# Kernel tuning notes

Measured on AMD Instinct MI355X. Metric: run time of the kernel, lower is better.

The kernel has to match this reference:

```python
import jax, jax.numpy as jnp
import numpy as np

B, S, DIM = 2, 4096, 768
G = DIM // 3          # gate_dim = 256
H, DK = 4, G // 4     # heads=4, d_k=64
SCALE = 1.0 / np.sqrt(DK)


def setup_inputs() -> dict:
    key = jax.random.key(0)
    ks = jax.random.split(key, 9)
    r = lambda k, shp, s: (jax.random.normal(k, shp, dtype=jnp.float32) * s)
    w_s = 1.0 / np.sqrt(G)
    return {
        "x": r(ks[0], (B, S, DIM), 1.0),
        "wq": r(ks[1], (G, G), w_s), "bq": r(ks[2], (G,), 0.01),
        "wk": r(ks[3], (G, G), w_s), "bk": r(ks[4], (G,), 0.01),
        "wv": r(ks[5], (G, G), w_s), "bv": r(ks[6], (G,), 0.01),
        "wo": r(ks[7], (G, G), w_s), "bo": r(ks[8], (G,), 0.01),
    }


def reference(x, wq, bq, wk, bk, wv, bv, wo, bo):
    # chunk(3, dim=-1): q/k/v slices of width G
    xq, xk, xv = x[..., :G], x[..., G:2 * G], x[..., 2 * G:3 * G]
    # linear projections then split into heads: [b, s, h, d]
    q = (xq @ wq.T + bq).reshape(B, S, H, DK)
    k = (xk @ wk.T + bk).reshape(B, S, H, DK)
    v = (xv @ wv.T + bv).reshape(B, S, H, DK)
    scores = jnp.einsum('bihd,bjhd->bijh', q, k) * SCALE  # [b, i, j, h]
    # NOTE: original applies Softmax(dim=1) -> over the QUERY axis i
    attn = jax.nn.softmax(scores, axis=1)
    out = jnp.einsum('bijh,bjhd->bihd', attn, v).reshape(B, S, G)
    return out @ wo.T + bo
```

## Files before the change

kernel.cpp:

```cpp
#include <hip/hip_runtime.h>

#define SEQ   4096
#define HH    4
#define SCALE 0.125f

typedef __bf16 bf16x8 __attribute__((ext_vector_type(8)));
typedef __bf16 bf16x4 __attribute__((ext_vector_type(4)));
typedef float  f32x4  __attribute__((ext_vector_type(4)));

constexpr size_t OFF_W16  = 0;
constexpr size_t OFF_A    = 131072;
constexpr size_t OFF_PZ   = 163840;
constexpr size_t OFF_AO   = 294912;
constexpr size_t OFF_X16  = 9732096;
constexpr size_t OFF_Q16  = 12877824;
constexpr size_t K16OFF   = 2097152;
constexpr size_t V16OFF   = 4194304;

__device__ __forceinline__ f32x4 mf(bf16x8 a, bf16x8 b, f32x4 c) {
    return __builtin_amdgcn_mfma_f32_16x16x32_bf16(a, b, c, 0, 0, 0);
}

__device__ __forceinline__ void gload16(const __bf16* g, __bf16* l) {
    __builtin_amdgcn_global_load_lds(
        (const __attribute__((address_space(1))) unsigned int*)g,
        (__attribute__((address_space(3))) unsigned int*)l, 16, 0, 0);
}

__global__ void k_prep(const float* __restrict__ x,
                       const float* __restrict__ wq, const float* __restrict__ wk,
                       const float* __restrict__ wv, const float* __restrict__ wo,
                       float* __restrict__ ws) {
    int bx = blockIdx.x, t = threadIdx.x;
    if (bx < 6144) {
        size_t i4 = ((size_t)bx * 256 + t) * 4;
        float4 v = *(const float4*)(x + i4);
        bf16x4 o = {(__bf16)v.x, (__bf16)v.y, (__bf16)v.z, (__bf16)v.w};
        *(bf16x4*)((__bf16*)(ws + OFF_X16) + i4) = o;
    } else if (bx < 6400) {
        int q = bx - 6144;
        int y = q >> 6;
        const float* src = (y == 0) ? wq : (y == 1) ? wk : (y == 2) ? wv : wo;
        size_t i4 = ((size_t)(q & 63) * 256 + t) * 4;
        float4 v = *(const float4*)(src + i4);
        bf16x4 o = {(__bf16)v.x, (__bf16)v.y, (__bf16)v.z, (__bf16)v.w};
        *(bf16x4*)((__bf16*)(ws + OFF_W16) + (size_t)y * 65536 + i4) = o;
    } else {
        size_t i4 = ((size_t)(bx - 6400) * 256 + t) * 4;
        *(float4*)(ws + OFF_AO + i4) = make_float4(0.f, 0.f, 0.f, 0.f);
    }
}

__global__ __launch_bounds__(256) void k_qkv_mfma(const float* __restrict__ bq,
                                                  const float* __restrict__ bk,
                                                  const float* __restrict__ bv,
                                                  float* __restrict__ ws) {
    int t = threadIdx.x, lane = t & 63, w = t >> 6;
    int yw = blockIdx.y;
    int row0 = blockIdx.x * 64 + w * 16;
    int mrow = lane & 15, quad = lane >> 4;
    const __bf16* X16 = (const __bf16*)(ws + OFF_X16);
    const __bf16* W16 = (const __bf16*)(ws + OFF_W16) + (size_t)yw * 65536;
    const float* bias = (yw == 0) ? bq : (yw == 1) ? bk : bv;
    __bf16* Qb = (__bf16*)(ws + OFF_Q16);
    f32x4 acc[16];
#pragma unroll
    for (int n = 0; n < 16; n++) acc[n] = {0.f, 0.f, 0.f, 0.f};
    const __bf16* ap = X16 + (size_t)(row0 + mrow) * 768 + yw * 256 + quad * 8;
    const __bf16* bp = W16 + (size_t)mrow * 256 + quad * 8;
    for (int kc = 0; kc < 256; kc += 32) {
        bf16x8 a = *(const bf16x8*)(ap + kc);
#pragma unroll
        for (int nt = 0; nt < 16; nt++) {
            bf16x8 b = *(const bf16x8*)(bp + (size_t)nt * 16 * 256 + kc);
            acc[nt] = mf(a, b, acc[nt]);
        }
    }
#pragma unroll
    for (int nt = 0; nt < 16; nt++) {
        int n = nt * 16 + mrow;
        float bb = bias[n];
        int h = n >> 6, d = n & 63;
#pragma unroll
        for (int r = 0; r < 4; r++) {
            int sg = row0 + quad * 4 + r;
            int b_ = sg >> 12, s = sg & 4095;
            int bh = b_ * HH + h;
            float val = acc[nt][r] + bb;
            if (yw <= 1) {
                int tile = s >> 4, m = s & 15, frag = d >> 5, q2 = (d >> 3) & 3, e = d & 7;
                size_t idx = (((size_t)bh * 256 + tile) * 2 + frag) * 512 +
                             (size_t)(q2 * 16 + m) * 8 + e;
                ((yw == 0) ? Qb : Qb + K16OFF)[idx] = (__bf16)val;
            } else {
                int jc = s >> 5, qk = (s >> 3) & 3, e = s & 7;
                int nd = d >> 4, nl = d & 15;
                size_t idx = (((size_t)bh * 128 + jc) * 4 + nd) * 512 +
                             (size_t)(qk * 16 + nl) * 8 + e;
                Qb[V16OFF + idx] = (__bf16)val;
            }
        }
    }
}

__global__ __launch_bounds__(256) void k_colstats(float* __restrict__ ws) {
    __shared__ __bf16 qbuf[2][4096];
    int t = threadIdx.x, lane = t & 63, w = t >> 6;
    int jb = blockIdx.x, iy = blockIdx.y, bh = blockIdx.z;
    int jt0 = jb * 8 + w * 2;
    const __bf16* Qp = (const __bf16*)(ws + OFF_Q16);
    const __bf16* Kp = Qp + K16OFF;
    const __bf16* kb = Kp + (((size_t)bh * 256 + jt0) * 2) * 512 + lane * 8;
    bf16x8 bk00 = *(const bf16x8*)(kb);
    bf16x8 bk01 = *(const bf16x8*)(kb + 512);
    bf16x8 bk10 = *(const bf16x8*)(kb + 1024);
    bf16x8 bk11 = *(const bf16x8*)(kb + 1536);
    const __bf16* q0 = Qp + (((size_t)bh * 256 + iy * 64) * 2) * 512 +
                       w * 1024 + lane * 8;
    gload16(q0, qbuf[0] + w * 1024);
    gload16(q0 + 512, qbuf[0] + w * 1024 + 512);
    __syncthreads();
    float z0 = 0.f, z1 = 0.f;
    for (int ic = 0; ic < 16; ic++) {
        const __bf16* cur = qbuf[ic & 1];
        if (ic < 15) {
            const __bf16* qn = Qp + (((size_t)bh * 256 + iy * 64 + (ic + 1) * 4) * 2) * 512 +
                               w * 1024 + lane * 8;
            gload16(qn, qbuf[(ic + 1) & 1] + w * 1024);
            gload16(qn + 512, qbuf[(ic + 1) & 1] + w * 1024 + 512);
        }
#pragma unroll
        for (int it = 0; it < 4; it++) {
            bf16x8 a0 = *(const bf16x8*)(cur + it * 1024 + lane * 8);
            bf16x8 a1 = *(const bf16x8*)(cur + it * 1024 + 512 + lane * 8);
            f32x4 c0 = {0.f, 0.f, 0.f, 0.f};
            c0 = mf(a0, bk00, c0);
            c0 = mf(a1, bk01, c0);
            f32x4 c1 = {0.f, 0.f, 0.f, 0.f};
            c1 = mf(a0, bk10, c1);
            c1 = mf(a1, bk11, c1);
#pragma unroll
            for (int r = 0; r < 4; r++) {
                z0 += __expf(fmaf(c0[r], SCALE, -16.0f));
                z1 += __expf(fmaf(c1[r], SCALE, -16.0f));
            }
        }
        __syncthreads();
    }
    z0 += __shfl_xor(z0, 16, 64);
    z0 += __shfl_xor(z0, 32, 64);
    z1 += __shfl_xor(z1, 16, 64);
    z1 += __shfl_xor(z1, 32, 64);
    if (lane < 16) {
        size_t o = OFF_PZ + (size_t)iy * 32768 + (size_t)bh * SEQ + jt0 * 16 + lane;
        ws[o] = z0;
        ws[o + 16] = z1;
    }
}

__global__ void k_afin(float* __restrict__ ws) {
    int idx = blockIdx.x * 256 + threadIdx.x;
    const float* pz = ws + OFF_PZ;
    float Z = pz[idx] + pz[32768 + (size_t)idx] + pz[65536 + (size_t)idx] +
              pz[98304 + (size_t)idx];
    ws[OFF_A + idx] = -16.0f - __logf(Z);
}

__global__ __launch_bounds__(256) void k_attnpv(float* __restrict__ ws) {
    __shared__ __bf16 ldsK[2][2048], ldsV[2][2048], ptile[4 * 1280];
    int t = threadIdx.x, lane = t & 63, w = t >> 6;
    int jy = blockIdx.y, bh = blockIdx.z;
    int it0 = blockIdx.x * 8 + w * 2;
    int mrow = lane & 15, quad = lane >> 4;
    const __bf16* Qp = (const __bf16*)(ws + OFF_Q16);
    const __bf16* Kp = Qp + K16OFF;
    const __bf16* Vp = Qp + V16OFF;
    const float* Ac = ws + OFF_A + (size_t)bh * SEQ;
    __bf16* pt = ptile + w * 1280;

    const __bf16* qb = Qp + (((size_t)bh * 256 + it0) * 2) * 512 + lane * 8;
    bf16x8 aq00 = *(const bf16x8*)(qb);
    bf16x8 aq01 = *(const bf16x8*)(qb + 512);
    bf16x8 aq10 = *(const bf16x8*)(qb + 1024);
    bf16x8 aq11 = *(const bf16x8*)(qb + 1536);

    f32x4 oacc[2][4];
#pragma unroll
    for (int tt = 0; tt < 2; tt++)
#pragma unroll
        for (int nd = 0; nd < 4; nd++) oacc[tt][nd] = {0.f, 0.f, 0.f, 0.f};

    int jbase = jy * 1024;
    {
        const __bf16* kg = Kp + (((size_t)bh * 256 + (jbase >> 4)) * 2) * 512 +
                           w * 512 + lane * 8;
        gload16(kg, ldsK[0] + w * 512);
        const __bf16* vg = Vp + (((size_t)bh * 128 + (jbase >> 5)) * 4) * 512 +
                           w * 512 + lane * 8;
        gload16(vg, ldsV[0] + w * 512);
    }
    __syncthreads();

    for (int jt = 0; jt < 32; jt++) {
        int j0 = jbase + jt * 32;
        const __bf16* curK = ldsK[jt & 1];
        const __bf16* curV = ldsV[jt & 1];
        if (jt < 31) {
            int jn = j0 + 32;
            const __bf16* kg = Kp + (((size_t)bh * 256 + (jn >> 4)) * 2) * 512 +
                               w * 512 + lane * 8;
            gload16(kg, ldsK[(jt + 1) & 1] + w * 512);
            const __bf16* vg = Vp + (((size_t)bh * 128 + (jn >> 5)) * 4) * 512 +
                               w * 512 + lane * 8;
            gload16(vg, ldsV[(jt + 1) & 1] + w * 512);
        }
        float ca0 = Ac[j0 + mrow], ca1 = Ac[j0 + 16 + mrow];
        bf16x8 ck0 = *(const bf16x8*)(curK + lane * 8);
        bf16x8 ck1 = *(const bf16x8*)(curK + 512 + lane * 8);
        bf16x8 ck2 = *(const bf16x8*)(curK + 1024 + lane * 8);
        bf16x8 ck3 = *(const bf16x8*)(curK + 1536 + lane * 8);
#pragma unroll
        for (int tt = 0; tt < 2; tt++) {
            bf16x8 a0 = tt ? aq10 : aq00;
            bf16x8 a1 = tt ? aq11 : aq01;
            f32x4 c0 = {0.f, 0.f, 0.f, 0.f};
            c0 = mf(a0, ck0, c0);
            c0 = mf(a1, ck1, c0);
            f32x4 c1 = {0.f, 0.f, 0.f, 0.f};
            c1 = mf(a0, ck2, c1);
            c1 = mf(a1, ck3, c1);
#pragma unroll
            for (int r = 0; r < 4; r++) {
                float p0 = __expf(fmaf(c0[r], SCALE, ca0));
                pt[(tt * 16 + quad * 4 + r) * 40 + mrow] = (__bf16)p0;
                float p1 = __expf(fmaf(c1[r], SCALE, ca1));
                pt[(tt * 16 + quad * 4 + r) * 40 + 16 + mrow] = (__bf16)p1;
            }
        }
        bf16x8 ap0 = *(const bf16x8*)(pt + mrow * 40 + quad * 8);
        bf16x8 ap1 = *(const bf16x8*)(pt + (16 + mrow) * 40 + quad * 8);
#pragma unroll
        for (int nd = 0; nd < 4; nd++) {
            bf16x8 bv = *(const bf16x8*)(curV + nd * 512 + lane * 8);
            oacc[0][nd] = mf(ap0, bv, oacc[0][nd]);
            oacc[1][nd] = mf(ap1, bv, oacc[1][nd]);
        }
        __syncthreads();
    }

    int b = bh >> 2, h = bh & 3;
    float* AO = ws + OFF_AO;
#pragma unroll
    for (int tt = 0; tt < 2; tt++) {
#pragma unroll
        for (int nd = 0; nd < 4; nd++) {
#pragma unroll
            for (int r = 0; r < 4; r++) {
                int i = (it0 + tt) * 16 + quad * 4 + r;
                int d = nd * 16 + mrow;
                atomicAdd(&AO[((size_t)(b * SEQ + i)) * 256 + h * 64 + d],
                          oacc[tt][nd][r]);
            }
        }
    }
}

__global__ __launch_bounds__(256) void k_outproj_mfma(const float* __restrict__ bo,
                                                      float* __restrict__ ws,
                                                      float* __restrict__ out) {
    int t = threadIdx.x, lane = t & 63, w = t >> 6;
    int row0 = blockIdx.x * 64 + w * 16;
    int mrow = lane & 15, quad = lane >> 4;
    const float* AO = ws + OFF_AO;
    const __bf16* W16 = (const __bf16*)(ws + OFF_W16) + (size_t)3 * 65536;
    f32x4 acc[16];
#pragma unroll
    for (int n = 0; n < 16; n++) acc[n] = {0.f, 0.f, 0.f, 0.f};
    const float* ap = AO + (size_t)(row0 + mrow) * 256 + quad * 8;
    const __bf16* bp = W16 + (size_t)mrow * 256 + quad * 8;
    for (int kc = 0; kc < 256; kc += 32) {
        float4 u = *(const float4*)(ap + kc);
        float4 v = *(const float4*)(ap + kc + 4);
        bf16x8 a = {(__bf16)u.x, (__bf16)u.y, (__bf16)u.z, (__bf16)u.w,
                    (__bf16)v.x, (__bf16)v.y, (__bf16)v.z, (__bf16)v.w};
#pragma unroll
        for (int nt = 0; nt < 16; nt++) {
            bf16x8 b = *(const bf16x8*)(bp + (size_t)nt * 16 * 256 + kc);
            acc[nt] = mf(a, b, acc[nt]);
        }
    }
#pragma unroll
    for (int nt = 0; nt < 16; nt++) {
        int n = nt * 16 + mrow;
        float bb = bo[n];
#pragma unroll
        for (int r = 0; r < 4; r++) {
            int sg = row0 + quad * 4 + r;
            out[(size_t)sg * 256 + n] = acc[nt][r] + bb;
        }
    }
}

extern "C" void kernel_launch(void* const* d_in, const int* in_sizes, int n_in,
                              void* d_out, int out_size, void* d_ws, size_t ws_size,
                              hipStream_t stream) {
    const float* x  = (const float*)d_in[0];
    const float* wq = (const float*)d_in[1];
    const float* bq = (const float*)d_in[2];
    const float* wk = (const float*)d_in[3];
    const float* bk = (const float*)d_in[4];
    const float* wv = (const float*)d_in[5];
    const float* bv = (const float*)d_in[6];
    const float* wo = (const float*)d_in[7];
    const float* bo = (const float*)d_in[8];
    float* ws = (float*)d_ws;
    float* out = (float*)d_out;

    k_prep<<<8448, 256, 0, stream>>>(x, wq, wk, wv, wo, ws);
    k_qkv_mfma<<<dim3(128, 3), 256, 0, stream>>>(bq, bk, bv, ws);
    k_colstats<<<dim3(32, 4, 8), 256, 0, stream>>>(ws);
    k_afin<<<128, 256, 0, stream>>>(ws);
    k_attnpv<<<dim3(32, 4, 8), 256, 0, stream>>>(ws);
    k_outproj_mfma<<<128, 256, 0, stream>>>(bo, ws, out);
}
```

Before: 247.5 us.

## Transpose attention MFMA to keep P in registers, re-layout K, use exp2

The PV kernel now computes the transposed score tile K·Qᵀ, so the exponentiated probabilities land directly in the MFMA operand layout. This removes the LDS round trip for the P tile, and K is stored in a permuted layout to match. Column statistics and the probabilities use exp2 with a log2e-prescaled constant, and column-normalization values are staged in LDS. Grids are also retuned: colstats now has 8 i-splits, and attnpv uses one 16-row tile per wave with twice as many blocks. The output is written back through LDS so atomic adds are coalesced. The costs are more blocks re-streaming K/V and more partial sums for Z.

```diff
diff --git a/kernel.cpp b/kernel.cpp
--- a/kernel.cpp
+++ b/kernel.cpp
@@ -3,6 +3,8 @@
 #define SEQ   4096
 #define HH    4
 #define SCALE 0.125f
+#define SC2   0.18033688011112042f
+#define C16   -23.083120654223414f
 
 typedef __bf16 bf16x8 __attribute__((ext_vector_type(8)));
 typedef __bf16 bf16x4 __attribute__((ext_vector_type(4)));
@@ -10,12 +12,12 @@
 
 constexpr size_t OFF_W16  = 0;
 constexpr size_t OFF_A    = 131072;
-constexpr size_t OFF_PZ   = 163840;
 constexpr size_t OFF_AO   = 294912;
 constexpr size_t OFF_X16  = 9732096;
 constexpr size_t OFF_Q16  = 12877824;
 constexpr size_t K16OFF   = 2097152;
 constexpr size_t V16OFF   = 4194304;
+constexpr size_t OFF_PZ   = 16023552;
 
 __device__ __forceinline__ f32x4 mf(bf16x8 a, bf16x8 b, f32x4 c) {
     return __builtin_amdgcn_mfma_f32_16x16x32_bf16(a, b, c, 0, 0, 0);
@@ -25,6 +27,10 @@
     __builtin_amdgcn_global_load_lds(
         (const __attribute__((address_space(1))) unsigned int*)g,
         (__attribute__((address_space(3))) unsigned int*)l, 16, 0, 0);
+}
+
+__device__ __forceinline__ float ex2(float x) {
+    return __builtin_amdgcn_exp2f(x);
 }
 
 __global__ void k_prep(const float* __restrict__ x,
@@ -87,11 +93,18 @@
             int b_ = sg >> 12, s = sg & 4095;
             int bh = b_ * HH + h;
             float val = acc[nt][r] + bb;
-            if (yw <= 1) {
+            if (yw == 0) {
                 int tile = s >> 4, m = s & 15, frag = d >> 5, q2 = (d >> 3) & 3, e = d & 7;
                 size_t idx = (((size_t)bh * 256 + tile) * 2 + frag) * 512 +
                              (size_t)(q2 * 16 + m) * 8 + e;
-                ((yw == 0) ? Qb : Qb + K16OFF)[idx] = (__bf16)val;
+                Qb[idx] = (__bf16)val;
+            } else if (yw == 1) {
+                int jc = s >> 5, jj = s & 31;
+                int tl = (jj >> 2) & 1, m = ((jj >> 3) << 2) | (jj & 3);
+                int frag = d >> 5, q2 = (d >> 3) & 3, e = d & 7;
+                size_t idx = (((size_t)bh * 128 + jc) * 4 + tl * 2 + frag) * 512 +
+                             (size_t)(q2 * 16 + m) * 8 + e;
+                Qb[K16OFF + idx] = (__bf16)val;
             } else {
                 int jc = s >> 5, qk = (s >> 3) & 3, e = s & 7;
                 int nd = d >> 4, nl = d & 15;
@@ -107,24 +120,24 @@
     __shared__ __bf16 qbuf[2][4096];
     int t = threadIdx.x, lane = t & 63, w = t >> 6;
     int jb = blockIdx.x, iy = blockIdx.y, bh = blockIdx.z;
-    int jt0 = jb * 8 + w * 2;
+    int jc = jb * 4 + w;
     const __bf16* Qp = (const __bf16*)(ws + OFF_Q16);
     const __bf16* Kp = Qp + K16OFF;
-    const __bf16* kb = Kp + (((size_t)bh * 256 + jt0) * 2) * 512 + lane * 8;
+    const __bf16* kb = Kp + ((size_t)(bh * 128 + jc) * 4) * 512 + lane * 8;
     bf16x8 bk00 = *(const bf16x8*)(kb);
     bf16x8 bk01 = *(const bf16x8*)(kb + 512);
     bf16x8 bk10 = *(const bf16x8*)(kb + 1024);
     bf16x8 bk11 = *(const bf16x8*)(kb + 1536);
-    const __bf16* q0 = Qp + (((size_t)bh * 256 + iy * 64) * 2) * 512 +
+    const __bf16* q0 = Qp + ((size_t)(bh * 256 + iy * 32) * 2) * 512 +
                        w * 1024 + lane * 8;
     gload16(q0, qbuf[0] + w * 1024);
     gload16(q0 + 512, qbuf[0] + w * 1024 + 512);
     __syncthreads();
     float z0 = 0.f, z1 = 0.f;
-    for (int ic = 0; ic < 16; ic++) {
+    for (int ic = 0; ic < 8; ic++) {
         const __bf16* cur = qbuf[ic & 1];
-        if (ic < 15) {
-            const __bf16* qn = Qp + (((size_t)bh * 256 + iy * 64 + (ic + 1) * 4) * 2) * 512 +
+        if (ic < 7) {
+            const __bf16* qn = Qp + ((size_t)(bh * 256 + iy * 32 + (ic + 1) * 4) * 2) * 512 +
                                w * 1024 + lane * 8;
             gload16(qn, qbuf[(ic + 1) & 1] + w * 1024);
             gload16(qn + 512, qbuf[(ic + 1) & 1] + w * 1024 + 512);
@@ -141,8 +154,8 @@
             c1 = mf(a1, bk11, c1);
 #pragma unroll
             for (int r = 0; r < 4; r++) {
-                z0 += __expf(fmaf(c0[r], SCALE, -16.0f));
-                z1 += __expf(fmaf(c1[r], SCALE, -16.0f));
+                z0 += ex2(fmaf(c0[r], SC2, C16));
+                z1 += ex2(fmaf(c1[r], SC2, C16));
             }
         }
         __syncthreads();
@@ -152,116 +165,103 @@
     z1 += __shfl_xor(z1, 16, 64);
     z1 += __shfl_xor(z1, 32, 64);
     if (lane < 16) {
-        size_t o = OFF_PZ + (size_t)iy * 32768 + (size_t)bh * SEQ + jt0 * 16 + lane;
+        size_t o = OFF_PZ + (size_t)iy * 32768 + (size_t)bh * SEQ +
+                   jc * 32 + ((lane >> 2) << 3) + (lane & 3);
         ws[o] = z0;
-        ws[o + 16] = z1;
+        ws[o + 4] = z1;
     }
 }
 
 __global__ void k_afin(float* __restrict__ ws) {
     int idx = blockIdx.x * 256 + threadIdx.x;
     const float* pz = ws + OFF_PZ;
-    float Z = pz[idx] + pz[32768 + (size_t)idx] + pz[65536 + (size_t)idx] +
-              pz[98304 + (size_t)idx];
-    ws[OFF_A + idx] = -16.0f - __logf(Z);
+    float Z = 0.f;
+#pragma unroll
+    for (int y = 0; y < 8; y++) Z += pz[(size_t)y * 32768 + idx];
+    ws[OFF_A + idx] = C16 - __log2f(Z);
 }
 
 __global__ __launch_bounds__(256) void k_attnpv(float* __restrict__ ws) {
-    __shared__ __bf16 ldsK[2][2048], ldsV[2][2048], ptile[4 * 1280];
+    __shared__ __align__(16) char pool[20480];
+    __bf16* ldsK = (__bf16*)pool;
+    __bf16* ldsV = (__bf16*)(pool + 8192);
+    float*  sA   = (float*)(pool + 16384);
     int t = threadIdx.x, lane = t & 63, w = t >> 6;
     int jy = blockIdx.y, bh = blockIdx.z;
-    int it0 = blockIdx.x * 8 + w * 2;
+    int it0 = blockIdx.x * 4 + w;
+    int i0 = it0 * 16;
     int mrow = lane & 15, quad = lane >> 4;
     const __bf16* Qp = (const __bf16*)(ws + OFF_Q16);
     const __bf16* Kp = Qp + K16OFF;
     const __bf16* Vp = Qp + V16OFF;
-    const float* Ac = ws + OFF_A + (size_t)bh * SEQ;
-    __bf16* pt = ptile + w * 1280;
-
-    const __bf16* qb = Qp + (((size_t)bh * 256 + it0) * 2) * 512 + lane * 8;
-    bf16x8 aq00 = *(const bf16x8*)(qb);
-    bf16x8 aq01 = *(const bf16x8*)(qb + 512);
-    bf16x8 aq10 = *(const bf16x8*)(qb + 1024);
-    bf16x8 aq11 = *(const bf16x8*)(qb + 1536);
-
-    f32x4 oacc[2][4];
-#pragma unroll
-    for (int tt = 0; tt < 2; tt++)
-#pragma unroll
-        for (int nd = 0; nd < 4; nd++) oacc[tt][nd] = {0.f, 0.f, 0.f, 0.f};
-
     int jbase = jy * 1024;
     {
-        const __bf16* kg = Kp + (((size_t)bh * 256 + (jbase >> 4)) * 2) * 512 +
-                           w * 512 + lane * 8;
-        gload16(kg, ldsK[0] + w * 512);
-        const __bf16* vg = Vp + (((size_t)bh * 128 + (jbase >> 5)) * 4) * 512 +
-                           w * 512 + lane * 8;
-        gload16(vg, ldsV[0] + w * 512);
+        const float* Ag = ws + OFF_A + (size_t)bh * SEQ + jbase;
+        *(float4*)(sA + t * 4) = *(const float4*)(Ag + t * 4);
+    }
+    const __bf16* qb = Qp + ((size_t)(bh * 256 + it0) * 2) * 512 + lane * 8;
+    bf16x8 aq0 = *(const bf16x8*)(qb);
+    bf16x8 aq1 = *(const bf16x8*)(qb + 512);
+    f32x4 oaccT[4];
+#pragma unroll
+    for (int nd = 0; nd < 4; nd++) oaccT[nd] = {0.f, 0.f, 0.f, 0.f};
+    int c0g = jy * 32;
+    {
+        const __bf16* kg = Kp + ((size_t)(bh * 128 + c0g) * 4) * 512 + w * 512 + lane * 8;
+        gload16(kg, ldsK + w * 512);
+        const __bf16* vg = Vp + ((size_t)(bh * 128 + c0g) * 4) * 512 + w * 512 + lane * 8;
+        gload16(vg, ldsV + w * 512);
     }
     __syncthreads();
 
     for (int jt = 0; jt < 32; jt++) {
-        int j0 = jbase + jt * 32;
-        const __bf16* curK = ldsK[jt & 1];
-        const __bf16* curV = ldsV[jt & 1];
+        const __bf16* curK = ldsK + (jt & 1) * 2048;
+        const __bf16* curV = ldsV + (jt & 1) * 2048;
         if (jt < 31) {
-            int jn = j0 + 32;
-            const __bf16* kg = Kp + (((size_t)bh * 256 + (jn >> 4)) * 2) * 512 +
-                               w * 512 + lane * 8;
-            gload16(kg, ldsK[(jt + 1) & 1] + w * 512);
-            const __bf16* vg = Vp + (((size_t)bh * 128 + (jn >> 5)) * 4) * 512 +
-                               w * 512 + lane * 8;
-            gload16(vg, ldsV[(jt + 1) & 1] + w * 512);
-        }
-        float ca0 = Ac[j0 + mrow], ca1 = Ac[j0 + 16 + mrow];
+            int cn = c0g + jt + 1;
+            const __bf16* kg = Kp + ((size_t)(bh * 128 + cn) * 4) * 512 + w * 512 + lane * 8;
+            gload16(kg, ldsK + ((jt + 1) & 1) * 2048 + w * 512);
+            const __bf16* vg = Vp + ((size_t)(bh * 128 + cn) * 4) * 512 + w * 512 + lane * 8;
+            gload16(vg, ldsV + ((jt + 1) & 1) * 2048 + w * 512);
+        }
+        f32x4 a4L = *(const f32x4*)(sA + jt * 32 + quad * 8);
+        f32x4 a4H = *(const f32x4*)(sA + jt * 32 + quad * 8 + 4);
         bf16x8 ck0 = *(const bf16x8*)(curK + lane * 8);
         bf16x8 ck1 = *(const bf16x8*)(curK + 512 + lane * 8);
         bf16x8 ck2 = *(const bf16x8*)(curK + 1024 + lane * 8);
         bf16x8 ck3 = *(const bf16x8*)(curK + 1536 + lane * 8);
-#pragma unroll
-        for (int tt = 0; tt < 2; tt++) {
-            bf16x8 a0 = tt ? aq10 : aq00;
-            bf16x8 a1 = tt ? aq11 : aq01;
-            f32x4 c0 = {0.f, 0.f, 0.f, 0.f};
-            c0 = mf(a0, ck0, c0);
-            c0 = mf(a1, ck1, c0);
-            f32x4 c1 = {0.f, 0.f, 0.f, 0.f};
-            c1 = mf(a0, ck2, c1);
-            c1 = mf(a1, ck3, c1);
-#pragma unroll
-            for (int r = 0; r < 4; r++) {
-                float p0 = __expf(fmaf(c0[r], SCALE, ca0));
-                pt[(tt * 16 + quad * 4 + r) * 40 + mrow] = (__bf16)p0;
-                float p1 = __expf(fmaf(c1[r], SCALE, ca1));
-                pt[(tt * 16 + quad * 4 + r) * 40 + 16 + mrow] = (__bf16)p1;
-            }
-        }
-        bf16x8 ap0 = *(const bf16x8*)(pt + mrow * 40 + quad * 8);
-        bf16x8 ap1 = *(const bf16x8*)(pt + (16 + mrow) * 40 + quad * 8);
+        f32x4 cT0 = {0.f, 0.f, 0.f, 0.f};
+        cT0 = mf(ck0, aq0, cT0);
+        cT0 = mf(ck1, aq1, cT0);
+        f32x4 cT1 = {0.f, 0.f, 0.f, 0.f};
+        cT1 = mf(ck2, aq0, cT1);
+        cT1 = mf(ck3, aq1, cT1);
+        bf16x8 pb;
+#pragma unroll
+        for (int r = 0; r < 4; r++) {
+            pb[r]     = (__bf16)ex2(fmaf(cT0[r], SC2, a4L[r]));
+            pb[4 + r] = (__bf16)ex2(fmaf(cT1[r], SC2, a4H[r]));
+        }
 #pragma unroll
         for (int nd = 0; nd < 4; nd++) {
             bf16x8 bv = *(const bf16x8*)(curV + nd * 512 + lane * 8);
-            oacc[0][nd] = mf(ap0, bv, oacc[0][nd]);
-            oacc[1][nd] = mf(ap1, bv, oacc[1][nd]);
+            oaccT[nd] = mf(bv, pb, oaccT[nd]);
         }
         __syncthreads();
     }
 
+    float* sO = (float*)pool + (size_t)w * (16 * 65);
+#pragma unroll
+    for (int nd = 0; nd < 4; nd++)
+#pragma unroll
+        for (int r = 0; r < 4; r++)
+            sO[mrow * 65 + nd * 16 + quad * 4 + r] = oaccT[nd][r];
     int b = bh >> 2, h = bh & 3;
     float* AO = ws + OFF_AO;
 #pragma unroll
-    for (int tt = 0; tt < 2; tt++) {
-#pragma unroll
-        for (int nd = 0; nd < 4; nd++) {
-#pragma unroll
-            for (int r = 0; r < 4; r++) {
-                int i = (it0 + tt) * 16 + quad * 4 + r;
-                int d = nd * 16 + mrow;
-                atomicAdd(&AO[((size_t)(b * SEQ + i)) * 256 + h * 64 + d],
-                          oacc[tt][nd][r]);
-            }
-        }
+    for (int c = 0; c < 16; c++) {
+        atomicAdd(&AO[((size_t)(b * SEQ + i0 + c)) * 256 + h * 64 + lane],
+                  sO[c * 65 + lane]);
     }
 }
 
@@ -318,8 +318,8 @@
 
     k_prep<<<8448, 256, 0, stream>>>(x, wq, wk, wv, wo, ws);
     k_qkv_mfma<<<dim3(128, 3), 256, 0, stream>>>(bq, bk, bv, ws);
-    k_colstats<<<dim3(32, 4, 8), 256, 0, stream>>>(ws);
+    k_colstats<<<dim3(32, 8, 8), 256, 0, stream>>>(ws);
     k_afin<<<128, 256, 0, stream>>>(ws);
-    k_attnpv<<<dim3(32, 4, 8), 256, 0, stream>>>(ws);
+    k_attnpv<<<dim3(64, 4, 8), 256, 0, stream>>>(ws);
     k_outproj_mfma<<<128, 256, 0, stream>>>(bo, ws, out);
 }
```

New measurement: 224.7 us. -9.2%, faster.
